# Kernel optimization log

Hardware: AMD Instinct MI355X
Metric: run time of the kernel (lower is better)

The kernel has to match this reference:

```python
import jax, jax.numpy as jnp
import numpy as np

B, N, M, D = 32, 1024, 1024, 128  # pairs, nodes in X-graph, nodes in Y-graph, feature dim


def setup_inputs() -> dict:
    key = jax.random.key(0)
    k0, k1, k2, k3 = jax.random.split(key, 4)
    return {
        "Xs": jax.random.normal(k0, (B, N, D), dtype=jnp.float32),
        "Ys": jax.random.normal(k1, (B, M, D), dtype=jnp.float32),
        "weights": jax.random.normal(k2, (B, N, D), dtype=jnp.float32),
        "A_w": jax.random.normal(k3, (D, D), dtype=jnp.float32) / np.sqrt(D).astype(np.float32),
        "A_b": jnp.zeros((D,), dtype=jnp.float32),
    }


def reference(Xs, Ys, weights, A_w, A_b):
    # coefficients = tanh(Linear(W))  -> [B, N, D]
    coeff = jnp.tanh(jnp.einsum("bnd,ed->bne", weights, A_w) + A_b)
    # affinity: softplus((X * coeff) @ Y^T) - 0.5  -> [B, N, M]
    s = jax.nn.softplus(jnp.einsum("bnd,bmd->bnm", Xs * coeff, Ys)) - 0.5
    # dual-direction attention
    a_x = jax.nn.softmax(s, axis=2)   # row softmax (dim=1 on [N,M])
    a_y = jax.nn.softmax(s, axis=1)   # col softmax (dim=0 on [N,M])
    attention_x = jnp.einsum("bnm,bmd->bnd", a_x, Ys)   # a_x @ Y
    attention_y = jnp.einsum("bnm,bnd->bmd", a_y, Xs)   # a_y^T @ X
    return attention_x, attention_y, s
```

## Files before the change

### kernel.cpp

```cpp
#include <hip/hip_runtime.h>
#include <hip/hip_bf16.h>

#define BB 32
#define NN 1024
#define MM 1024
#define DD 128

typedef __bf16 bf16;
typedef bf16 bf16x8 __attribute__((ext_vector_type(8)));
typedef bf16 bf16x4 __attribute__((ext_vector_type(4)));
typedef float f32x4 __attribute__((ext_vector_type(4)));

#define LOG2E 1.4426950408889634f
#define LN2   0.6931471805599453f
#define ESHIFT 30.5f
#define ESHIFT_C 5.6757e-14f

__device__ __forceinline__ bf16x8 ld8(const bf16* p) {
    return *reinterpret_cast<const bf16x8*>(p);
}

__device__ __forceinline__ bf16x8 cvt8(const float* p) {
    float4 a = reinterpret_cast<const float4*>(p)[0];
    float4 c = reinterpret_cast<const float4*>(p)[1];
    bf16x8 r;
    r[0]=(bf16)a.x; r[1]=(bf16)a.y; r[2]=(bf16)a.z; r[3]=(bf16)a.w;
    r[4]=(bf16)c.x; r[5]=(bf16)c.y; r[6]=(bf16)c.z; r[7]=(bf16)c.w;
    return r;
}

__global__ void k_prep(const float* __restrict__ Xs, const float* __restrict__ Ys,
                       bf16* __restrict__ Ysb, bf16* __restrict__ YsT,
                       bf16* __restrict__ XsT) {
    __shared__ float tile[32][129];
    int b = blockIdx.y;
    int yy = blockIdx.x;
    int isY = (yy < 32);
    int r0 = (yy & 31) * 32;
    const float* s = (isY ? Ys : Xs) + (size_t)b * 1024 * DD;
    int tid = threadIdx.x;
    int c4 = (tid & 31) * 4;
#pragma unroll
    for (int p = 0; p < 4; ++p) {
        int r = p * 8 + (tid >> 5);
        float4 v = *reinterpret_cast<const float4*>(s + (size_t)(r0 + r) * DD + c4);
        tile[r][c4] = v.x; tile[r][c4 + 1] = v.y; tile[r][c4 + 2] = v.z; tile[r][c4 + 3] = v.w;
        if (isY) {
            bf16x4 o; o[0] = (bf16)v.x; o[1] = (bf16)v.y; o[2] = (bf16)v.z; o[3] = (bf16)v.w;
            *reinterpret_cast<bf16x4*>(Ysb + (size_t)b * MM * DD + (size_t)(r0 + r) * DD + c4) = o;
        }
    }
    __syncthreads();
    bf16* dT = (isY ? YsT : XsT) + (size_t)b * DD * 1024;
    int c = tid >> 1, rh = (tid & 1) * 16;
    bf16x8 o0, o1;
#pragma unroll
    for (int j = 0; j < 8; ++j) o0[j] = (bf16)tile[rh + j][c];
#pragma unroll
    for (int j = 0; j < 8; ++j) o1[j] = (bf16)tile[rh + 8 + j][c];
    *reinterpret_cast<bf16x8*>(dT + (size_t)c * 1024 + r0 + rh) = o0;
    *reinterpret_cast<bf16x8*>(dT + (size_t)c * 1024 + r0 + rh + 8) = o1;
}

__global__ __launch_bounds__(256) void k_coeff(
    const float* __restrict__ Xs, const float* __restrict__ W,
    const float* __restrict__ Aw, const float* __restrict__ Ab,
    bf16* __restrict__ Xc) {
    int ntile = blockIdx.x, b = blockIdx.y;
    int tid = threadIdx.x;
    int w = tid >> 6, lane = tid & 63, quad = lane >> 4, l16 = lane & 15;
    int nbase = ntile * 64 + w * 16;

    f32x4 accZ[8];
#pragma unroll
    for (int ef = 0; ef < 8; ++ef) accZ[ef] = {0.f, 0.f, 0.f, 0.f};

    const float* Wb = W + ((size_t)b * NN + nbase + l16) * DD;
#pragma unroll
    for (int ks = 0; ks < 4; ++ks) {
        bf16x8 aW = cvt8(Wb + ks * 32 + quad * 8);
#pragma unroll
        for (int ef = 0; ef < 8; ++ef) {
            bf16x8 bA = cvt8(Aw + (size_t)(ef * 16 + l16) * DD + ks * 32 + quad * 8);
            accZ[ef] = __builtin_amdgcn_mfma_f32_16x16x32_bf16(aW, bA, accZ[ef], 0, 0, 0);
        }
    }
#pragma unroll
    for (int ef = 0; ef < 8; ++ef) {
        float ab = Ab[ef * 16 + l16];
#pragma unroll
        for (int r = 0; r < 4; ++r) {
            float z = accZ[ef][r] + ab;
            z = fminf(fmaxf(z, -12.f), 12.f);
            float t = __builtin_amdgcn_exp2f(z * (2.f * LOG2E));
            float c = (t - 1.f) / (t + 1.f);
            int n = nbase + quad * 4 + r;
            size_t idx = ((size_t)b * NN + n) * DD + ef * 16 + l16;
            Xc[idx] = (bf16)(Xs[idx] * c);
        }
    }
}

__global__ __launch_bounds__(256, 2) void k_main(
    const bf16* __restrict__ Xc, const bf16* __restrict__ Ysb,
    const bf16* __restrict__ YsT, const bf16* __restrict__ XsT,
    float* __restrict__ out_x, float* __restrict__ out_y,
    float* __restrict__ out_s) {
    __shared__ __align__(16) bf16 stage[2][16384];
    __shared__ __align__(16) bf16 Et[4][16][72];

    int L = blockIdx.x + 32 * blockIdx.y;
    int xcd = L & 7, sidx = L >> 3;
    int b = xcd + 8 * (sidx & 3);
    int t = sidx >> 2;
    int role = t >> 4, tile = t & 15;
    int tid = threadIdx.x;
    int w = tid >> 6, lane = tid & 63, quad = lane >> 4, l16 = lane & 15;
    int rbase = tile * 64 + w * 16;

    const bf16* Arow  = (role == 0 ? Xc : Ysb) + ((size_t)b * 1024 + rbase + l16) * DD;
    const bf16* Bmat  = (role == 0 ? Ysb : Xc) + (size_t)b * 1024 * DD;
    const bf16* BTmat = (role == 0 ? YsT : XsT) + (size_t)b * DD * 1024;
    float* s_b = out_s + (size_t)b * NN * MM;
    float* outp = (role == 0 ? out_x : out_y);

    bf16x8 aX[4];
#pragma unroll
    for (int ks = 0; ks < 4; ++ks) aX[ks] = ld8(Arow + ks * 32 + quad * 8);

    int isA = (w < 2);
    uint32_t wroff[8];
    uint32_t soff[8];
#pragma unroll
    for (int i = 0; i < 8; ++i) {
        uint32_t o = (uint32_t)(w * 8 + i) * 1024 + (uint32_t)lane * 16;
        if (isA) {
            wroff[i] = o ^ (((o >> 8) & 7) << 4);
            soff[i]  = o;
        } else {
            uint32_t j = o - 16384;
            wroff[i] = 16384 + (j ^ (((j >> 7) & 7) << 4));
            soff[i]  = (j >> 7) * 2048 + (j & 127);
        }
    }
    const char* srcbase = (const char*)(isA ? Bmat : BTmat);
    uint32_t tstride = isA ? 16384u : 128u;

    bf16x8 stg[8];
#pragma unroll
    for (int i = 0; i < 8; ++i)
        stg[i] = *reinterpret_cast<const bf16x8*>(srcbase + soff[i]);
#pragma unroll
    for (int i = 0; i < 8; ++i)
        *reinterpret_cast<bf16x8*>((char*)&stage[0][0] + wroff[i]) = stg[i];
    __syncthreads();

    f32x4 accU[8];
#pragma unroll
    for (int df = 0; df < 8; ++df) accU[df] = {0.f, 0.f, 0.f, 0.f};
    float rowsum[4] = {0.f, 0.f, 0.f, 0.f};
    uint32_t xq = (uint32_t)(l16 & 7) << 4;
    int cur = 0;

#pragma unroll 1
    for (int tt = 0; tt < 16; ++tt) {
        if (tt < 15) {
#pragma unroll
            for (int i = 0; i < 8; ++i)
                stg[i] = *reinterpret_cast<const bf16x8*>(srcbase + (size_t)(tt + 1) * tstride + soff[i]);
        }
        __builtin_amdgcn_sched_barrier(0);

        const char* sb = (const char*)&stage[cur][0];
        f32x4 accS[4];
#pragma unroll
        for (int mf = 0; mf < 4; ++mf) accS[mf] = {0.f, 0.f, 0.f, 0.f};
#pragma unroll
        for (int ks = 0; ks < 4; ++ks) {
            bf16x8 bY[4];
#pragma unroll
            for (int mf = 0; mf < 4; ++mf)
                bY[mf] = *reinterpret_cast<const bf16x8*>(
                    sb + (uint32_t)(mf * 16 + l16) * 256 + (((uint32_t)(ks * 64 + quad * 16)) ^ xq));
#pragma unroll
            for (int mf = 0; mf < 4; ++mf)
                accS[mf] = __builtin_amdgcn_mfma_f32_16x16x32_bf16(aX[ks], bY[mf], accS[mf], 0, 0, 0);
        }
#pragma unroll
        for (int mf = 0; mf < 4; ++mf) {
#pragma unroll
            for (int r = 0; r < 4; ++r) {
                float x = accS[mf][r];
                float E = __builtin_amdgcn_exp2f((x - ESHIFT) * LOG2E) + ESHIFT_C;
                bf16 Eb = (bf16)E;
                rowsum[r] += (float)Eb;
                Et[w][quad * 4 + r][mf * 16 + l16] = Eb;
            }
            if (role == 0) {
#pragma unroll
                for (int r = 0; r < 4; ++r) {
                    float x = accS[mf][r];
                    float ax = fabsf(x);
                    float sp = fmaxf(x, 0.f) +
                               LN2 * __builtin_amdgcn_logf(1.f + __builtin_amdgcn_exp2f(-ax * LOG2E));
                    s_b[(size_t)(rbase + quad * 4 + r) * MM + tt * 64 + mf * 16 + l16] = sp - 0.5f;
                }
            }
        }
#pragma unroll
        for (int half = 0; half < 2; ++half) {
            bf16x8 aE = *reinterpret_cast<const bf16x8*>(&Et[w][l16][half * 32 + quad * 8]);
            bf16x8 bT[8];
#pragma unroll
            for (int df = 0; df < 8; ++df)
                bT[df] = *reinterpret_cast<const bf16x8*>(
                    sb + 16384 + (uint32_t)(df * 16 + l16) * 128 + (((uint32_t)(half * 64 + quad * 16)) ^ xq));
#pragma unroll
            for (int df = 0; df < 8; ++df)
                accU[df] = __builtin_amdgcn_mfma_f32_16x16x32_bf16(aE, bT[df], accU[df], 0, 0, 0);
        }
        __builtin_amdgcn_sched_barrier(0);
        if (tt < 15) {
#pragma unroll
            for (int i = 0; i < 8; ++i)
                *reinterpret_cast<bf16x8*>((char*)&stage[cur ^ 1][0] + wroff[i]) = stg[i];
        }
        __syncthreads();
        cur ^= 1;
    }

    float inv[4];
#pragma unroll
    for (int r = 0; r < 4; ++r) {
        float rs = rowsum[r];
        rs += __shfl_xor(rs, 1); rs += __shfl_xor(rs, 2);
        rs += __shfl_xor(rs, 4); rs += __shfl_xor(rs, 8);
        inv[r] = 1.f / rs;
    }
#pragma unroll
    for (int df = 0; df < 8; ++df)
#pragma unroll
        for (int r = 0; r < 4; ++r)
            outp[((size_t)b * 1024 + rbase + quad * 4 + r) * DD + df * 16 + l16] = accU[df][r] * inv[r];
}

extern "C" void kernel_launch(void* const* d_in, const int* in_sizes, int n_in,
                              void* d_out, int out_size, void* d_ws, size_t ws_size,
                              hipStream_t stream) {
    const float* Xs = (const float*)d_in[0];
    const float* Ys = (const float*)d_in[1];
    const float* W  = (const float*)d_in[2];
    const float* Aw = (const float*)d_in[3];
    const float* Ab = (const float*)d_in[4];

    char* ws = (char*)d_ws;
    bf16*  Xc     = (bf16*)(ws);
    bf16*  Ysb    = (bf16*)(ws + 8388608);
    bf16*  YsT    = (bf16*)(ws + 16777216);
    bf16*  XsT    = (bf16*)(ws + 25165824);

    float* out_x = (float*)d_out;
    float* out_y = out_x + (size_t)BB * NN * DD;
    float* out_s = out_y + (size_t)BB * MM * DD;

    k_prep<<<dim3(64, BB), 256, 0, stream>>>(Xs, Ys, Ysb, YsT, XsT);
    k_coeff<<<dim3(NN / 64, BB), 256, 0, stream>>>(Xs, W, Aw, Ab, Xc);
    k_main<<<dim3(32, BB), 256, 0, stream>>>(Xc, Ysb, YsT, XsT, out_x, out_y, out_s);
}
```

Before: 294.3 us.

## Merge prep and coeff kernels, single-buffer main stage for higher occupancy

Folds the transpose/convert prep kernel and the coefficient GEMM kernel into one launch, with blocks split by role, and changes the transpose tiling to 128x32 tiles. In the main kernel the double-buffered LDS stage becomes a single buffer with an extra barrier before each refill, and launch bounds rise to three blocks per SIMD group. The goal is fewer launches and more resident blocks to hide latency. The cost is an added sync per iteration, which serialises compute against the LDS writes, and possible register pressure.

Result: slower. 349.1 us (+18.6%).

```diff
diff --git a/kernel.cpp b/kernel.cpp
--- a/kernel.cpp
+++ b/kernel.cpp
@@ -29,84 +29,84 @@
     return r;
 }
 
-__global__ void k_prep(const float* __restrict__ Xs, const float* __restrict__ Ys,
-                       bf16* __restrict__ Ysb, bf16* __restrict__ YsT,
-                       bf16* __restrict__ XsT) {
-    __shared__ float tile[32][129];
-    int b = blockIdx.y;
-    int yy = blockIdx.x;
-    int isY = (yy < 32);
-    int r0 = (yy & 31) * 32;
-    const float* s = (isY ? Ys : Xs) + (size_t)b * 1024 * DD;
+__global__ __launch_bounds__(256) void k_pre(
+    const float* __restrict__ Xs, const float* __restrict__ Ys,
+    const float* __restrict__ W, const float* __restrict__ Aw,
+    const float* __restrict__ Ab, bf16* __restrict__ Xc,
+    bf16* __restrict__ Ysb, bf16* __restrict__ YsT, bf16* __restrict__ XsT) {
+    __shared__ float tile[128][35];
+    int bx = blockIdx.x, b = blockIdx.y;
     int tid = threadIdx.x;
-    int c4 = (tid & 31) * 4;
+
+    if (bx < 16) {
+        int w = tid >> 6, lane = tid & 63, quad = lane >> 4, l16 = lane & 15;
+        int nbase = bx * 64 + w * 16;
+        f32x4 accZ[8];
+#pragma unroll
+        for (int ef = 0; ef < 8; ++ef) accZ[ef] = {0.f, 0.f, 0.f, 0.f};
+        const float* Wb = W + ((size_t)b * NN + nbase + l16) * DD;
+#pragma unroll
+        for (int ks = 0; ks < 4; ++ks) {
+            bf16x8 aW = cvt8(Wb + ks * 32 + quad * 8);
+#pragma unroll
+            for (int ef = 0; ef < 8; ++ef) {
+                bf16x8 bA = cvt8(Aw + (size_t)(ef * 16 + l16) * DD + ks * 32 + quad * 8);
+                accZ[ef] = __builtin_amdgcn_mfma_f32_16x16x32_bf16(aW, bA, accZ[ef], 0, 0, 0);
+            }
+        }
+#pragma unroll
+        for (int ef = 0; ef < 8; ++ef) {
+            float ab = Ab[ef * 16 + l16];
+#pragma unroll
+            for (int r = 0; r < 4; ++r) {
+                float z = accZ[ef][r] + ab;
+                z = fminf(fmaxf(z, -12.f), 12.f);
+                float t = __builtin_amdgcn_exp2f(z * (2.f * LOG2E));
+                float c = (t - 1.f) / (t + 1.f);
+                int n = nbase + quad * 4 + r;
+                size_t idx = ((size_t)b * NN + n) * DD + ef * 16 + l16;
+                Xc[idx] = (bf16)(Xs[idx] * c);
+            }
+        }
+        return;
+    }
+
+    int s = bx - 16;
+    int isY = (s < 32) ? 1 : 0;
+    s &= 31;
+    int mtile = s >> 2, dtile = s & 3;
+    int r0 = mtile * 128, d0 = dtile * 32;
+    const float* src = (isY ? Ys : Xs) + (size_t)b * 1024 * DD;
 #pragma unroll
     for (int p = 0; p < 4; ++p) {
-        int r = p * 8 + (tid >> 5);
-        float4 v = *reinterpret_cast<const float4*>(s + (size_t)(r0 + r) * DD + c4);
-        tile[r][c4] = v.x; tile[r][c4 + 1] = v.y; tile[r][c4 + 2] = v.z; tile[r][c4 + 3] = v.w;
+        int row = p * 32 + (tid >> 3);
+        int c = (tid & 7) * 4;
+        float4 v = *reinterpret_cast<const float4*>(src + (size_t)(r0 + row) * DD + d0 + c);
+        tile[row][c] = v.x; tile[row][c + 1] = v.y; tile[row][c + 2] = v.z; tile[row][c + 3] = v.w;
         if (isY) {
             bf16x4 o; o[0] = (bf16)v.x; o[1] = (bf16)v.y; o[2] = (bf16)v.z; o[3] = (bf16)v.w;
-            *reinterpret_cast<bf16x4*>(Ysb + (size_t)b * MM * DD + (size_t)(r0 + r) * DD + c4) = o;
+            *reinterpret_cast<bf16x4*>(Ysb + (size_t)b * MM * DD + (size_t)(r0 + row) * DD + d0 + c) = o;
         }
     }
     __syncthreads();
     bf16* dT = (isY ? YsT : XsT) + (size_t)b * DD * 1024;
-    int c = tid >> 1, rh = (tid & 1) * 16;
+    int dd = tid >> 3;
+    int mseg = (tid & 7) * 16;
     bf16x8 o0, o1;
 #pragma unroll
-    for (int j = 0; j < 8; ++j) o0[j] = (bf16)tile[rh + j][c];
-#pragma unroll
-    for (int j = 0; j < 8; ++j) o1[j] = (bf16)tile[rh + 8 + j][c];
-    *reinterpret_cast<bf16x8*>(dT + (size_t)c * 1024 + r0 + rh) = o0;
-    *reinterpret_cast<bf16x8*>(dT + (size_t)c * 1024 + r0 + rh + 8) = o1;
-}
-
-__global__ __launch_bounds__(256) void k_coeff(
-    const float* __restrict__ Xs, const float* __restrict__ W,
-    const float* __restrict__ Aw, const float* __restrict__ Ab,
-    bf16* __restrict__ Xc) {
-    int ntile = blockIdx.x, b = blockIdx.y;
-    int tid = threadIdx.x;
-    int w = tid >> 6, lane = tid & 63, quad = lane >> 4, l16 = lane & 15;
-    int nbase = ntile * 64 + w * 16;
-
-    f32x4 accZ[8];
-#pragma unroll
-    for (int ef = 0; ef < 8; ++ef) accZ[ef] = {0.f, 0.f, 0.f, 0.f};
-
-    const float* Wb = W + ((size_t)b * NN + nbase + l16) * DD;
-#pragma unroll
-    for (int ks = 0; ks < 4; ++ks) {
-        bf16x8 aW = cvt8(Wb + ks * 32 + quad * 8);
-#pragma unroll
-        for (int ef = 0; ef < 8; ++ef) {
-            bf16x8 bA = cvt8(Aw + (size_t)(ef * 16 + l16) * DD + ks * 32 + quad * 8);
-            accZ[ef] = __builtin_amdgcn_mfma_f32_16x16x32_bf16(aW, bA, accZ[ef], 0, 0, 0);
-        }
-    }
-#pragma unroll
-    for (int ef = 0; ef < 8; ++ef) {
-        float ab = Ab[ef * 16 + l16];
-#pragma unroll
-        for (int r = 0; r < 4; ++r) {
-            float z = accZ[ef][r] + ab;
-            z = fminf(fmaxf(z, -12.f), 12.f);
-            float t = __builtin_amdgcn_exp2f(z * (2.f * LOG2E));
-            float c = (t - 1.f) / (t + 1.f);
-            int n = nbase + quad * 4 + r;
-            size_t idx = ((size_t)b * NN + n) * DD + ef * 16 + l16;
-            Xc[idx] = (bf16)(Xs[idx] * c);
-        }
-    }
-}
-
-__global__ __launch_bounds__(256, 2) void k_main(
+    for (int j = 0; j < 8; ++j) o0[j] = (bf16)tile[mseg + j][dd];
+#pragma unroll
+    for (int j = 0; j < 8; ++j) o1[j] = (bf16)tile[mseg + 8 + j][dd];
+    *reinterpret_cast<bf16x8*>(dT + (size_t)(d0 + dd) * 1024 + r0 + mseg) = o0;
+    *reinterpret_cast<bf16x8*>(dT + (size_t)(d0 + dd) * 1024 + r0 + mseg + 8) = o1;
+}
+
+__global__ __launch_bounds__(256, 3) void k_main(
     const bf16* __restrict__ Xc, const bf16* __restrict__ Ysb,
     const bf16* __restrict__ YsT, const bf16* __restrict__ XsT,
     float* __restrict__ out_x, float* __restrict__ out_y,
     float* __restrict__ out_s) {
-    __shared__ __align__(16) bf16 stage[2][16384];
+    __shared__ __align__(16) bf16 stage[16384];
     __shared__ __align__(16) bf16 Et[4][16][72];
 
     int L = blockIdx.x + 32 * blockIdx.y;
@@ -129,8 +129,7 @@
     for (int ks = 0; ks < 4; ++ks) aX[ks] = ld8(Arow + ks * 32 + quad * 8);
 
     int isA = (w < 2);
-    uint32_t wroff[8];
-    uint32_t soff[8];
+    uint32_t wroff[8], soff[8];
 #pragma unroll
     for (int i = 0; i < 8; ++i) {
         uint32_t o = (uint32_t)(w * 8 + i) * 1024 + (uint32_t)lane * 16;
@@ -152,7 +151,7 @@
         stg[i] = *reinterpret_cast<const bf16x8*>(srcbase + soff[i]);
 #pragma unroll
     for (int i = 0; i < 8; ++i)
-        *reinterpret_cast<bf16x8*>((char*)&stage[0][0] + wroff[i]) = stg[i];
+        *reinterpret_cast<bf16x8*>((char*)&stage[0] + wroff[i]) = stg[i];
     __syncthreads();
 
     f32x4 accU[8];
@@ -160,7 +159,6 @@
     for (int df = 0; df < 8; ++df) accU[df] = {0.f, 0.f, 0.f, 0.f};
     float rowsum[4] = {0.f, 0.f, 0.f, 0.f};
     uint32_t xq = (uint32_t)(l16 & 7) << 4;
-    int cur = 0;
 
 #pragma unroll 1
     for (int tt = 0; tt < 16; ++tt) {
@@ -171,7 +169,7 @@
         }
         __builtin_amdgcn_sched_barrier(0);
 
-        const char* sb = (const char*)&stage[cur][0];
+        const char* sb = (const char*)&stage[0];
         f32x4 accS[4];
 #pragma unroll
         for (int mf = 0; mf < 4; ++mf) accS[mf] = {0.f, 0.f, 0.f, 0.f};
@@ -219,14 +217,13 @@
             for (int df = 0; df < 8; ++df)
                 accU[df] = __builtin_amdgcn_mfma_f32_16x16x32_bf16(aE, bT[df], accU[df], 0, 0, 0);
         }
-        __builtin_amdgcn_sched_barrier(0);
+        __syncthreads();
         if (tt < 15) {
 #pragma unroll
             for (int i = 0; i < 8; ++i)
-                *reinterpret_cast<bf16x8*>((char*)&stage[cur ^ 1][0] + wroff[i]) = stg[i];
+                *reinterpret_cast<bf16x8*>((char*)&stage[0] + wroff[i]) = stg[i];
         }
         __syncthreads();
-        cur ^= 1;
     }
 
     float inv[4];
@@ -263,7 +260,6 @@
     float* out_y = out_x + (size_t)BB * NN * DD;
     float* out_s = out_y + (size_t)BB * MM * DD;
 
-    k_prep<<<dim3(64, BB), 256, 0, stream>>>(Xs, Ys, Ysb, YsT, XsT);
-    k_coeff<<<dim3(NN / 64, BB), 256, 0, stream>>>(Xs, W, Aw, Ab, Xc);
+    k_pre<<<dim3(80, BB), 256, 0, stream>>>(Xs, Ys, W, Aw, Ab, Xc, Ysb, YsT, XsT);
     k_main<<<dim3(32, BB), 256, 0, stream>>>(Xc, Ysb, YsT, XsT, out_x, out_y, out_s);
 }
```
